# Kernel optimization log

Measured on AMD Instinct MI355X. Metric: run time of the kernel, lower is better.

Reference implementation:

```python
import jax, jax.numpy as jnp
import numpy as np

N_NODES = 50000

def _spmm(edge_index, edge_weight, feat):
    # adj @ feat where adj is given as COO edge list (dst <- src)
    src = edge_index[1]
    dst = edge_index[0]
    msgs = feat[src] * edge_weight[:, None]  # [E, F]
    return jax.ops.segment_sum(msgs, dst, num_segments=N_NODES)

def setup_inputs() -> dict:
    key = jax.random.key(0)
    ks = jax.random.split(key, 8)
    E = 1600000
    x = jax.random.normal(ks[0], (N_NODES, 512), dtype=jnp.float32)
    edge_index = jax.random.randint(ks[1], (2, E), 0, N_NODES, dtype=jnp.int32)
    edge_weight = jax.random.uniform(ks[2], (E,), dtype=jnp.float32)
    # Glorot-ish init like GraphConvolution.reset_parameters
    W1 = jax.random.normal(ks[3], (512, 128), dtype=jnp.float32) / np.sqrt(512)
    b1 = jax.random.normal(ks[4], (128,), dtype=jnp.float32) * 0.01
    W2 = jax.random.normal(ks[5], (128, 64), dtype=jnp.float32) / np.sqrt(128)
    b2 = jax.random.normal(ks[6], (64,), dtype=jnp.float32) * 0.01
    return {"x": x, "edge_index": edge_index, "edge_weight": edge_weight,
            "W1": W1, "b1": b1, "W2": W2, "b2": b2}

def reference(x, edge_index, edge_weight, W1, b1, W2, b2):
    # eval mode: F.dropout is identity when not training
    # gc1: adj @ (x @ W1) + b1, then relu
    support1 = x @ W1                                   # [N, nhid]
    x1 = jax.nn.relu(_spmm(edge_index, edge_weight, support1) + b1)
    # gc2: adj @ (x1 @ W2) + b2
    support2 = x1 @ W2                                  # [N, out]
    x2 = _spmm(edge_index, edge_weight, support2) + b2
    return (x1, x2)
```

## Files before the change

### kernel.cpp

```cpp
#include <hip/hip_runtime.h>
#include <hip/hip_bf16.h>

#define N_NODES 50000
#define N_EDGES 1600000
#define F_IN    512
#define F_HID   128
#define F_OUT   64
#define NBUK    391
#define EPB     8192
#define CAP     4864

typedef short bf16x8 __attribute__((ext_vector_type(8)));
typedef float f32x4  __attribute__((ext_vector_type(4)));

__device__ __forceinline__ short f32_to_bf16(float f) {
    unsigned u = __float_as_uint(f);
    u += 0x7FFF + ((u >> 16) & 1);
    return (short)(u >> 16);
}
__device__ __forceinline__ float bf16_to_f32(short s) {
    return __uint_as_float(((unsigned)(unsigned short)s) << 16);
}
__device__ __forceinline__ float bf16lo(unsigned u) { return __uint_as_float(u << 16); }
__device__ __forceinline__ float bf16hi(unsigned u) { return __uint_as_float(u & 0xFFFF0000u); }

__device__ __forceinline__ bf16x8 cvt8(float4 lo, float4 hi) {
    union { unsigned u[4]; bf16x8 v; } r;
    asm("v_cvt_pk_bf16_f32 %0, %1, %2" : "=v"(r.u[0]) : "v"(lo.x), "v"(lo.y));
    asm("v_cvt_pk_bf16_f32 %0, %1, %2" : "=v"(r.u[1]) : "v"(lo.z), "v"(lo.w));
    asm("v_cvt_pk_bf16_f32 %0, %1, %2" : "=v"(r.u[2]) : "v"(hi.x), "v"(hi.y));
    asm("v_cvt_pk_bf16_f32 %0, %1, %2" : "=v"(r.u[3]) : "v"(hi.z), "v"(hi.w));
    return r.v;
}

__device__ __forceinline__ void gload16(const void* g, void* l) {
    __builtin_amdgcn_global_load_lds((const __attribute__((address_space(1))) void*)g,
                                     (__attribute__((address_space(3))) void*)l, 16, 0, 0);
}


__global__ __launch_bounds__(256) void part_a(const int* __restrict__ dst,
                                              const int* __restrict__ src,
                                              const float* __restrict__ w,
                                              int* __restrict__ gcnt,
                                              uint2* __restrict__ tmp, int E) {
    __shared__ int h[NBUK];
    __shared__ int base[NBUK];
    for (int i = threadIdx.x; i < NBUK; i += 256) h[i] = 0;
    __syncthreads();
    int e0 = blockIdx.x * EPB;
    int e1 = min(e0 + EPB, E);
    for (int e = e0 + threadIdx.x; e < e1; e += 256)
        atomicAdd(&h[dst[e] >> 7], 1);
    __syncthreads();
    for (int i = threadIdx.x; i < NBUK; i += 256) {
        int c = h[i];
        base[i] = c ? atomicAdd(&gcnt[i], c) : 0;
        h[i] = 0;
    }
    __syncthreads();
    for (int e = e0 + threadIdx.x; e < e1; e += 256) {
        int d = dst[e];
        int b = d >> 7;
        int off = base[b] + atomicAdd(&h[b], 1);
        if (off < CAP)
            tmp[(size_t)b * CAP + off] = make_uint2(((unsigned)d << 16) | (unsigned)src[e],
                                                    __float_as_uint(w[e]));
    }
}

__global__ __launch_bounds__(256) void part_b(const uint2* __restrict__ tmp,
                                              const int* __restrict__ gcnt,
                                              int2* __restrict__ rowinfo,
                                              uint2* __restrict__ erec) {
    __shared__ int s[128];
    __shared__ int cur[128];
    int b = blockIdx.x, tid = threadIdx.x;
    int nb0 = b << 7;
    int r0 = b * CAP;
    int cnt_b = min(gcnt[b], CAP);
    int r1 = r0 + cnt_b;
    if (tid < 128) s[tid] = 0;
    __syncthreads();
    for (int i = r0 + tid; i < r1; i += 256)
        atomicAdd(&s[(tmp[i].x >> 16) - nb0], 1);
    __syncthreads();
    int v = (tid < 128) ? s[tid] : 0;
    #pragma unroll
    for (int off = 1; off < 128; off <<= 1) {
        int t = (tid >= off && tid < 128) ? s[tid - off] : 0;
        __syncthreads();
        if (tid < 128) s[tid] += t;
        __syncthreads();
    }
    if (tid < 128) {
        int ex = r0 + s[tid] - v;
        cur[tid] = ex;
        int node = nb0 + tid;
        if (node < N_NODES) rowinfo[node] = make_int2(ex, ex + v);
    }
    __syncthreads();
    for (int i = r0 + tid; i < r1; i += 256) {
        uint2 rec = tmp[i];
        int p = atomicAdd(&cur[(rec.x >> 16) - nb0], 1);
        erec[p] = make_uint2(rec.x & 0xFFFFu, rec.y);
    }
}


template<int KD, int NC>
__device__ __forceinline__ void wtrans_one(const float* __restrict__ W,
                                           bf16x8* __restrict__ Bfrag, int u) {
    constexpr int NT = NC / 16;
    int lane = u & 63;
    int nt   = (u >> 6) % NT;
    int kc   = u / (64 * NT);
    int n = nt * 16 + (lane & 15);
    int k = kc * 32 + (lane >> 4) * 8;
    bf16x8 f;
    #pragma unroll
    for (int j = 0; j < 8; ++j) f[j] = f32_to_bf16(W[(size_t)(k + j) * NC + n]);
    Bfrag[u] = f;
}

__global__ __launch_bounds__(256) void wtrans_all(const float* __restrict__ W1,
                                                  const float* __restrict__ W2,
                                                  bf16x8* __restrict__ B1,
                                                  bf16x8* __restrict__ B2) {
    constexpr int U1 = (F_IN / 32) * (F_HID / 16) * 64;
    constexpr int U2 = (F_HID / 32) * (F_OUT / 16) * 64;
    int u = blockIdx.x * 256 + threadIdx.x;
    if (u < U1) wtrans_one<F_IN, F_HID>(W1, B1, u);
    else if (u < U1 + U2) wtrans_one<F_HID, F_OUT>(W2, B2, u - U1);
}

template<int KD , int NC >
__global__ __launch_bounds__(256) void mfma_gemm_s1(const float* __restrict__ X,
                                                    const bf16x8* __restrict__ Bfrag,
                                                    short* __restrict__ C, int Mrows) {
    constexpr int S = KD / 32;
    __shared__ char lds[3][16384];
    const int tid  = threadIdx.x;
    const int lane = tid & 63;
    const int wave = tid >> 6;
    const int wm = wave >> 1, wn = wave & 1;
    const int B0 = blockIdx.x * 64;
    const int r_lo = lane & 15, cg = lane >> 4;

    int rowA = B0 + wave * 16 + r_lo;
    if (rowA > Mrows - 1) rowA = Mrows - 1;
    const char* gA = (const char*)(X + (size_t)rowA * KD) + cg * 32;
    const char* gB = (const char*)Bfrag + (size_t)(wave * 2) * 1024 + (size_t)lane * 16;

    const int dA0 = (0 * 256 + wave * 64) * 16;
    const int dA1 = (1 * 256 + wave * 64) * 16;
    const int dB0 = 8192 + (wave * 2 + 0) * 1024;
    const int dB1 = 8192 + (wave * 2 + 1) * 1024;

    f32x4 acc[2][4];
    #pragma unroll
    for (int m = 0; m < 2; ++m)
        #pragma unroll
        for (int n = 0; n < 4; ++n) acc[m][n] = (f32x4){0.f, 0.f, 0.f, 0.f};

    auto issue_stage = [&](int s, char* L) {
        const char* a = gA + (size_t)s * 128;
        const char* b = gB + (size_t)s * 8192;
        gload16(a,        L + dA0);
        gload16(a + 16,   L + dA1);
        gload16(b,        L + dB0);
        gload16(b + 1024, L + dB1);
    };
    auto compute_step = [&](const char* L) {
        const char* A_ = L;
        const char* B_ = L + 8192;
        bf16x8 bb[4];
        #pragma unroll
        for (int n = 0; n < 4; ++n)
            bb[n] = *(const bf16x8*)(B_ + (wn * 4 + n) * 1024 + lane * 16);
        #pragma unroll
        for (int m = 0; m < 2; ++m) {
            int t = wm * 2 + m;
            float4 lo = *(const float4*)(A_ + (0 * 256 + t * 64 + lane) * 16);
            float4 hi = *(const float4*)(A_ + (1 * 256 + t * 64 + lane) * 16);
            bf16x8 a = cvt8(lo, hi);
            #pragma unroll
            for (int n = 0; n < 4; ++n)
                acc[m][n] = __builtin_amdgcn_mfma_f32_16x16x32_bf16(a, bb[n], acc[m][n], 0, 0, 0);
        }
    };

    issue_stage(0, lds[0]);
    issue_stage(1, lds[1]);
    issue_stage(2, lds[2]);

    for (int s = 0; s < S - 2; ++s) {
        asm volatile("s_waitcnt vmcnt(8)" ::: "memory");
        asm volatile("s_barrier" ::: "memory");
        compute_step(lds[s % 3]);
        asm volatile("s_barrier" ::: "memory");
        if (s + 3 < S) issue_stage(s + 3, lds[s % 3]);
    }
    asm volatile("s_waitcnt vmcnt(4)" ::: "memory");
    asm volatile("s_barrier" ::: "memory");
    compute_step(lds[(S - 2) % 3]);
    asm volatile("s_waitcnt vmcnt(0)" ::: "memory");
    asm volatile("s_barrier" ::: "memory");
    compute_step(lds[(S - 1) % 3]);

    #pragma unroll
    for (int m = 0; m < 2; ++m) {
        int tile16 = (B0 >> 4) + wm * 2 + m;
        if (tile16 * 16 < Mrows) {
            #pragma unroll
            for (int n = 0; n < 4; ++n) {
                #pragma unroll
                for (int r = 0; r < 4; ++r) {
                    int grow = tile16 * 16 + cg * 4 + r;
                    C[(size_t)grow * NC + (wn * 4 + n) * 16 + r_lo] = f32_to_bf16(acc[m][n][r]);
                }
            }
        }
    }
}


template<int NC, int KD>
__global__ __launch_bounds__(256) void mfma_gemm_frag(const bf16x8* __restrict__ Afrag,
                                                      const bf16x8* __restrict__ Bfrag,
                                                      short* __restrict__ C, int Mt) {
    constexpr int NT = NC / 16, KC = KD / 32;
    constexpr int PFA = (KC < 4) ? KC : 4;
    const int lane = threadIdx.x & 63;
    const int wave = threadIdx.x >> 6;
    const int tile = blockIdx.x * 4 + wave;
    if (tile >= Mt) return;

    const bf16x8* ap = Afrag + (size_t)tile * KC * 64 + lane;
    const bf16x8* bp = Bfrag + lane;

    f32x4 acc[NT];
    #pragma unroll
    for (int i = 0; i < NT; ++i) acc[i] = (f32x4){0.f, 0.f, 0.f, 0.f};

    bf16x8 abuf[PFA];
    #pragma unroll
    for (int i = 0; i < PFA; ++i) abuf[i] = ap[(size_t)i * 64];
    bf16x8 bbuf[NT];
    #pragma unroll
    for (int nt = 0; nt < NT; ++nt) bbuf[nt] = bp[(size_t)nt * 64];

    #pragma unroll
    for (int kc = 0; kc < KC; ++kc) {
        bf16x8 a = abuf[kc % PFA];
        int ka = kc + PFA; if (ka > KC - 1) ka = KC - 1;
        abuf[kc % PFA] = ap[(size_t)ka * 64];
        int kb = (kc + 1 < KC) ? kc + 1 : kc;
        bf16x8 bnew[NT];
        #pragma unroll
        for (int nt = 0; nt < NT; ++nt) {
            bnew[nt] = bp[((size_t)kb * NT + nt) * 64];
            acc[nt] = __builtin_amdgcn_mfma_f32_16x16x32_bf16(a, bbuf[nt], acc[nt], 0, 0, 0);
        }
        #pragma unroll
        for (int nt = 0; nt < NT; ++nt) bbuf[nt] = bnew[nt];
    }

    const int lrow = lane & 15, kgrp = lane >> 4;
    #pragma unroll
    for (int nt = 0; nt < NT; ++nt) {
        #pragma unroll
        for (int r = 0; r < 4; ++r) {
            int grow = tile * 16 + kgrp * 4 + r;
            C[(size_t)grow * NC + nt * 16 + lrow] = f32_to_bf16(acc[nt][r]);
        }
    }
}


__global__ __launch_bounds__(64) void spmm128(const int2* __restrict__ rowinfo,
                                              const uint2* __restrict__ erec,
                                              const unsigned* __restrict__ featu,
                                              const float* __restrict__ bias,
                                              float* __restrict__ out,
                                              unsigned* __restrict__ afrag2u) {
    int d = blockIdx.x, tid = threadIdx.x;
    int2 ri = rowinfo[d];
    int beg = ri.x, end = ri.y;
    float a0 = 0.f, a1 = 0.f;
    const unsigned* fp = featu + tid;
    int e = beg;
    if (end - beg >= 8) {
        uint2 r[8];
        #pragma unroll
        for (int j = 0; j < 8; ++j) r[j] = erec[e + j];
        for (; e + 16 <= end; e += 8) {
            unsigned f[8];
            #pragma unroll
            for (int j = 0; j < 8; ++j) f[j] = fp[r[j].x * 64u];
            uint2 rn[8];
            #pragma unroll
            for (int j = 0; j < 8; ++j) rn[j] = erec[e + 8 + j];
            #pragma unroll
            for (int j = 0; j < 8; ++j) {
                float w = __uint_as_float(r[j].y);
                a0 += w * bf16lo(f[j]);
                a1 += w * bf16hi(f[j]);
            }
            #pragma unroll
            for (int j = 0; j < 8; ++j) r[j] = rn[j];
        }
        {
            unsigned f[8];
            #pragma unroll
            for (int j = 0; j < 8; ++j) f[j] = fp[r[j].x * 64u];
            #pragma unroll
            for (int j = 0; j < 8; ++j) {
                float w = __uint_as_float(r[j].y);
                a0 += w * bf16lo(f[j]);
                a1 += w * bf16hi(f[j]);
            }
            e += 8;
        }
    }
    for (; e + 4 <= end; e += 4) {
        uint2 r0 = erec[e], r1 = erec[e + 1], r2 = erec[e + 2], r3 = erec[e + 3];
        unsigned f0 = fp[r0.x * 64u];
        unsigned f1 = fp[r1.x * 64u];
        unsigned f2 = fp[r2.x * 64u];
        unsigned f3 = fp[r3.x * 64u];
        float w0 = __uint_as_float(r0.y), w1 = __uint_as_float(r1.y);
        float w2 = __uint_as_float(r2.y), w3 = __uint_as_float(r3.y);
        a0 += w0 * bf16lo(f0); a1 += w0 * bf16hi(f0);
        a0 += w1 * bf16lo(f1); a1 += w1 * bf16hi(f1);
        a0 += w2 * bf16lo(f2); a1 += w2 * bf16hi(f2);
        a0 += w3 * bf16lo(f3); a1 += w3 * bf16hi(f3);
    }
    for (; e < end; ++e) {
        uint2 r = erec[e];
        unsigned f = fp[r.x * 64u];
        float w = __uint_as_float(r.y);
        a0 += w * bf16lo(f); a1 += w * bf16hi(f);
    }
    float ox = fmaxf(a0 + bias[2 * tid], 0.f);
    float oy = fmaxf(a1 + bias[2 * tid + 1], 0.f);
    *(float2*)&out[(size_t)d * 128 + 2 * tid] = make_float2(ox, oy);
    unsigned packed = (unsigned)(unsigned short)f32_to_bf16(ox) |
                      ((unsigned)(unsigned short)f32_to_bf16(oy) << 16);
    int unit = ((d >> 4) * 4 + (tid >> 4)) * 64 + ((tid >> 2) & 3) * 16 + (d & 15);
    afrag2u[unit * 4 + (tid & 3)] = packed;
}

__global__ __launch_bounds__(64) void spmm64(const int2* __restrict__ rowinfo,
                                             const uint2* __restrict__ erec,
                                             const short* __restrict__ feat,
                                             const float* __restrict__ bias,
                                             float* __restrict__ out) {
    int d = blockIdx.x, tid = threadIdx.x;
    int2 ri = rowinfo[d];
    int beg = ri.x, end = ri.y;
    float acc = 0.f;
    const short* fp = feat + tid;
    int e = beg;
    if (end - beg >= 8) {
        uint2 r[8];
        #pragma unroll
        for (int j = 0; j < 8; ++j) r[j] = erec[e + j];
        for (; e + 16 <= end; e += 8) {
            float f[8];
            #pragma unroll
            for (int j = 0; j < 8; ++j) f[j] = bf16_to_f32(fp[r[j].x * 64u]);
            uint2 rn[8];
            #pragma unroll
            for (int j = 0; j < 8; ++j) rn[j] = erec[e + 8 + j];
            #pragma unroll
            for (int j = 0; j < 8; ++j) acc += __uint_as_float(r[j].y) * f[j];
            #pragma unroll
            for (int j = 0; j < 8; ++j) r[j] = rn[j];
        }
        {
            float f[8];
            #pragma unroll
            for (int j = 0; j < 8; ++j) f[j] = bf16_to_f32(fp[r[j].x * 64u]);
            #pragma unroll
            for (int j = 0; j < 8; ++j) acc += __uint_as_float(r[j].y) * f[j];
            e += 8;
        }
    }
    for (; e + 4 <= end; e += 4) {
        uint2 r0 = erec[e], r1 = erec[e + 1], r2 = erec[e + 2], r3 = erec[e + 3];
        float f0 = bf16_to_f32(fp[r0.x * 64u]);
        float f1 = bf16_to_f32(fp[r1.x * 64u]);
        float f2 = bf16_to_f32(fp[r2.x * 64u]);
        float f3 = bf16_to_f32(fp[r3.x * 64u]);
        acc += __uint_as_float(r0.y) * f0;
        acc += __uint_as_float(r1.y) * f1;
        acc += __uint_as_float(r2.y) * f2;
        acc += __uint_as_float(r3.y) * f3;
    }
    for (; e < end; ++e) {
        uint2 r = erec[e];
        acc += __uint_as_float(r.y) * bf16_to_f32(fp[r.x * 64u]);
    }
    out[(size_t)d * 64 + tid] = acc + bias[tid];
}


extern "C" void kernel_launch(void* const* d_in, const int* in_sizes, int n_in,
                              void* d_out, int out_size, void* d_ws, size_t ws_size,
                              hipStream_t stream) {
    const float* x  = (const float*)d_in[0];
    const int*   ei = (const int*)d_in[1];
    const float* ew = (const float*)d_in[2];
    const float* W1 = (const float*)d_in[3];
    const float* b1 = (const float*)d_in[4];
    const float* W2 = (const float*)d_in[5];
    const float* b2 = (const float*)d_in[6];

    const int* dst = ei;
    const int* src = ei + N_EDGES;

    float* x1 = (float*)d_out;
    float* x2 = x1 + (size_t)N_NODES * F_HID;

    char* ws = (char*)d_ws;
    uint2*  erec     = (uint2*)ws;  ws += (size_t)NBUK * CAP * 8;
    uint2*  tmp      = (uint2*)ws;  ws += (size_t)NBUK * CAP * 8;
    short*  support1 = (short*)ws;  ws += (size_t)N_NODES * F_HID * 2;
    short*  support2 = (short*)ws;  ws += (size_t)N_NODES * F_OUT * 2;
    bf16x8* Afrag2   = (bf16x8*)ws; ws += (size_t)N_NODES * F_HID * 2;
    bf16x8* Bfrag1   = (bf16x8*)ws; ws += (size_t)F_HID * F_IN * 2;
    bf16x8* Bfrag2   = (bf16x8*)ws; ws += (size_t)F_OUT * F_HID * 2;
    int2*   rowinfo  = (int2*)ws;   ws += (size_t)N_NODES * 8;
    int*    gcnt     = (int*)ws;    ws += 400 * 4;

    const int NPB = (N_EDGES + EPB - 1) / EPB;
    const int MT  = N_NODES / 16;

    hipMemsetAsync(gcnt, 0, NBUK * sizeof(int), stream);
    part_a<<<NPB, 256, 0, stream>>>(dst, src, ew, gcnt, tmp, N_EDGES);
    part_b<<<NBUK, 256, 0, stream>>>(tmp, gcnt, rowinfo, erec);

    wtrans_all<<<36, 256, 0, stream>>>(W1, W2, Bfrag1, Bfrag2);

    {
        int blocks = (N_NODES + 63) / 64;
        mfma_gemm_s1<F_IN, F_HID><<<blocks, 256, 0, stream>>>(x, Bfrag1, support1, N_NODES);
    }

    spmm128<<<N_NODES, 64, 0, stream>>>(rowinfo, erec, (const unsigned*)support1, b1, x1,
                                        (unsigned*)Afrag2);

    mfma_gemm_frag<F_OUT, F_HID><<<(MT + 3) / 4, 256, 0, stream>>>(Afrag2, Bfrag2, support2, MT);

    spmm64<<<N_NODES, 64, 0, stream>>>(rowinfo, erec, support2, b2, x2);
}
```

Baseline: 349.2 us.

## Stage bucketed edge scatter through LDS for coalesced global writes

The partitioning kernels now stage records in shared memory. part_a sorts each block's edges by bucket locally before writing them out, and part_b sorts within a bucket in LDS before writing erec contiguously. This replaces scattered uncoalesced global writes with mostly contiguous ones, and drops EPB to 2048 so the per-block LDS buffers fit. The cost is more LDS usage (part_b needs about 78KB), which lowers occupancy, plus extra barriers and a scan over 391 buckets in every block.

```diff
diff --git a/kernel.cpp b/kernel.cpp
--- a/kernel.cpp
+++ b/kernel.cpp
@@ -7,7 +7,7 @@
 #define F_HID   128
 #define F_OUT   64
 #define NBUK    391
-#define EPB     8192
+#define EPB     2048
 #define CAP     4864
 
 typedef short bf16x8 __attribute__((ext_vector_type(8)));
@@ -45,27 +45,54 @@
                                               int* __restrict__ gcnt,
                                               uint2* __restrict__ tmp, int E) {
     __shared__ int h[NBUK];
-    __shared__ int base[NBUK];
-    for (int i = threadIdx.x; i < NBUK; i += 256) h[i] = 0;
+    __shared__ int base_[NBUK];
+    __shared__ int ex[NBUK];
+    __shared__ int curz[NBUK];
+    __shared__ int   ldst[EPB];
+    __shared__ uint2 rec[EPB];
+    __shared__ int   tgt[EPB];
+    const int tid = threadIdx.x;
+    for (int i = tid; i < NBUK; i += 256) { h[i] = 0; curz[i] = 0; }
     __syncthreads();
     int e0 = blockIdx.x * EPB;
     int e1 = min(e0 + EPB, E);
-    for (int e = e0 + threadIdx.x; e < e1; e += 256)
-        atomicAdd(&h[dst[e] >> 7], 1);
-    __syncthreads();
-    for (int i = threadIdx.x; i < NBUK; i += 256) {
+    int cnt = e1 - e0;
+    for (int e = e0 + tid; e < e1; e += 256) {
+        int d = dst[e];
+        ldst[e - e0] = d;
+        atomicAdd(&h[d >> 7], 1);
+    }
+    __syncthreads();
+    for (int i = tid; i < NBUK; i += 256) {
         int c = h[i];
-        base[i] = c ? atomicAdd(&gcnt[i], c) : 0;
-        h[i] = 0;
-    }
-    __syncthreads();
-    for (int e = e0 + threadIdx.x; e < e1; e += 256) {
-        int d = dst[e];
+        base_[i] = c ? atomicAdd(&gcnt[i], c) : 0;
+        ex[i] = c;
+    }
+    __syncthreads();
+    for (int off = 1; off < NBUK; off <<= 1) {
+        int i0 = tid, i1 = tid + 256;
+        int t0 = 0, t1 = 0;
+        if (i0 < NBUK && i0 >= off) t0 = ex[i0 - off];
+        if (i1 < NBUK && i1 >= off) t1 = ex[i1 - off];
+        __syncthreads();
+        if (i0 < NBUK && i0 >= off) ex[i0] += t0;
+        if (i1 < NBUK && i1 >= off) ex[i1] += t1;
+        __syncthreads();
+    }
+    for (int e = e0 + tid; e < e1; e += 256) {
+        int d = ldst[e - e0];
         int b = d >> 7;
-        int off = base[b] + atomicAdd(&h[b], 1);
-        if (off < CAP)
-            tmp[(size_t)b * CAP + off] = make_uint2(((unsigned)d << 16) | (unsigned)src[e],
-                                                    __float_as_uint(w[e]));
+        int j0 = atomicAdd(&curz[b], 1);
+        int slot = ex[b] - h[b] + j0;
+        rec[slot] = make_uint2(((unsigned)d << 16) | (unsigned)src[e],
+                               __float_as_uint(w[e]));
+        int goff = base_[b] + j0;
+        tgt[slot] = (goff < CAP) ? b * CAP + goff : -1;
+    }
+    __syncthreads();
+    for (int i = tid; i < cnt; i += 256) {
+        int t = tgt[i];
+        if (t >= 0) tmp[t] = rec[i];
     }
 }
 
@@ -75,15 +102,19 @@
                                               uint2* __restrict__ erec) {
     __shared__ int s[128];
     __shared__ int cur[128];
+    __shared__ uint2 rec[CAP];
+    __shared__ uint2 ord[CAP];
     int b = blockIdx.x, tid = threadIdx.x;
     int nb0 = b << 7;
     int r0 = b * CAP;
     int cnt_b = min(gcnt[b], CAP);
-    int r1 = r0 + cnt_b;
     if (tid < 128) s[tid] = 0;
     __syncthreads();
-    for (int i = r0 + tid; i < r1; i += 256)
-        atomicAdd(&s[(tmp[i].x >> 16) - nb0], 1);
+    for (int i = tid; i < cnt_b; i += 256) {
+        uint2 r = tmp[r0 + i];
+        rec[i] = r;
+        atomicAdd(&s[(r.x >> 16) - nb0], 1);
+    }
     __syncthreads();
     int v = (tid < 128) ? s[tid] : 0;
     #pragma unroll
@@ -94,17 +125,20 @@
         __syncthreads();
     }
     if (tid < 128) {
-        int ex = r0 + s[tid] - v;
+        int ex = s[tid] - v;
         cur[tid] = ex;
         int node = nb0 + tid;
-        if (node < N_NODES) rowinfo[node] = make_int2(ex, ex + v);
-    }
-    __syncthreads();
-    for (int i = r0 + tid; i < r1; i += 256) {
-        uint2 rec = tmp[i];
-        int p = atomicAdd(&cur[(rec.x >> 16) - nb0], 1);
-        erec[p] = make_uint2(rec.x & 0xFFFFu, rec.y);
-    }
+        if (node < N_NODES) rowinfo[node] = make_int2(r0 + ex, r0 + ex + v);
+    }
+    __syncthreads();
+    for (int i = tid; i < cnt_b; i += 256) {
+        uint2 r = rec[i];
+        int p = atomicAdd(&cur[(r.x >> 16) - nb0], 1);
+        ord[p] = make_uint2(r.x & 0xFFFFu, r.y);
+    }
+    __syncthreads();
+    for (int i = tid; i < cnt_b; i += 256)
+        erec[r0 + i] = ord[i];
 }
 
 
```

Measured after the change: 333.0 us. 1.05x faster.
